# Performance work log

Hardware: AMD Instinct MI355X
Metric: run time of the kernel (lower is better)

Reference implementation:

```python
import jax, jax.numpy as jnp
import numpy as np

# SMPL constants
B, V, NJ, NB, NP, NJR = 256, 6890, 24, 10, 207, 43
PARENTS = np.array([0, 0, 0, 0, 1, 2, 3, 4, 5, 6, 7, 8, 9, 9, 9, 12, 13, 14, 16, 17, 18, 19, 20, 21])


def setup_inputs() -> dict:
    key = jax.random.key(0)
    ks = jax.random.split(key, 8)
    beta = jax.random.normal(ks[0], (B, NB), jnp.float32)
    theta = jax.random.normal(ks[1], (B, NJ * 3), jnp.float32)
    v_template = jax.random.normal(ks[2], (V, 3), jnp.float32)
    shapedirs = jax.random.normal(ks[3], (NB, V * 3), jnp.float32) * 0.01
    posedirs = jax.random.normal(ks[4], (NP, V * 3), jnp.float32) * 0.01
    jr = jax.random.uniform(ks[5], (NJ, V), jnp.float32)
    J_regressor = jr / jr.sum(axis=1, keepdims=True)
    jr2 = jax.random.uniform(ks[6], (NJR, V), jnp.float32)
    joint_regressor = jr2 / jr2.sum(axis=1, keepdims=True)
    w = jax.random.uniform(ks[7], (V, NJ), jnp.float32)
    w = w / w.sum(axis=1, keepdims=True)
    weights = jnp.broadcast_to(w[None], (B, V, NJ))  # tiled skinning weights, as in the torch buffer
    return dict(beta=beta, theta=theta, v_template=v_template, shapedirs=shapedirs,
                posedirs=posedirs, J_regressor=J_regressor,
                joint_regressor=joint_regressor, weights=weights)


def batch_rodrigues(theta):  # [N,3] axis-angle -> [N,3,3] rotation (via quaternion, HMR-style)
    angle = jnp.linalg.norm(theta + 1e-8, axis=1, keepdims=True)
    r = theta / angle
    half = angle * 0.5
    quat = jnp.concatenate([jnp.cos(half), jnp.sin(half) * r], axis=1)
    quat = quat / jnp.linalg.norm(quat, axis=1, keepdims=True)
    w, x, y, z = quat[:, 0], quat[:, 1], quat[:, 2], quat[:, 3]
    R = jnp.stack([
        1 - 2 * (y * y + z * z), 2 * (x * y - w * z), 2 * (x * z + w * y),
        2 * (x * y + w * z), 1 - 2 * (x * x + z * z), 2 * (y * z - w * x),
        2 * (x * z - w * y), 2 * (y * z + w * x), 1 - 2 * (x * x + y * y)], axis=1)
    return R.reshape(-1, 3, 3)


def batch_global_rigid_transformation(Rs, J):  # Rs [B,24,3,3], J [B,24,3]; rotate_base=True
    Rx = jnp.array([[1., 0., 0.], [0., -1., 0.], [0., 0., -1.]], dtype=Rs.dtype)
    root_R = jnp.matmul(Rs[:, 0], Rx)

    def make_A(R, t):  # [B,3,3],[B,3] -> [B,4,4]
        top = jnp.concatenate([R, t[:, :, None]], axis=2)
        bot = jnp.broadcast_to(jnp.array([0., 0., 0., 1.], dtype=R.dtype), (R.shape[0], 1, 4))
        return jnp.concatenate([top, bot], axis=1)

    res = [make_A(root_R, J[:, 0])]
    for i in range(1, NJ):  # fixed kinematic chain of 24 joints
        t = J[:, i] - J[:, PARENTS[i]]
        res.append(jnp.matmul(res[PARENTS[i]], make_A(Rs[:, i], t)))
    results = jnp.stack(res, axis=1)  # [B,24,4,4]
    J_transformed = results[:, :, :3, 3]
    Jh = jnp.concatenate([J, jnp.zeros_like(J[..., :1])], axis=-1)  # [B,24,4], w=0
    init_bone = jnp.einsum('bjmn,bjn->bjm', results, Jh)
    A = results - jnp.pad(init_bone[..., None], ((0, 0), (0, 0), (0, 0), (3, 0)))
    return J_transformed, A


def reference(beta, theta, v_template, shapedirs, posedirs, J_regressor, joint_regressor, weights):
    Bn = beta.shape[0]
    # shape blendshapes
    v_shaped = jnp.matmul(beta, shapedirs).reshape(Bn, V, 3) + v_template
    # joint locations from shaped mesh
    J = jnp.einsum('bvd,jv->bjd', v_shaped, J_regressor)  # [B,24,3]
    # pose rotations + pose blendshapes
    Rs = batch_rodrigues(theta.reshape(-1, 3)).reshape(Bn, NJ, 3, 3)
    pose_feature = (Rs[:, 1:] - jnp.eye(3, dtype=Rs.dtype)).reshape(Bn, NP)
    v_posed = jnp.matmul(pose_feature, posedirs).reshape(Bn, V, 3) + v_shaped
    # kinematic chain
    J_transformed, A = batch_global_rigid_transformation(Rs, J)
    # linear blend skinning
    T = jnp.einsum('bvj,bjmn->bvmn', weights, A)  # [B,V,4,4]
    vh = jnp.concatenate([v_posed, jnp.ones_like(v_posed[..., :1])], axis=-1)  # [B,V,4]
    verts = jnp.einsum('bvmn,bvn->bvm', T, vh)[..., :3]
    joints = jnp.einsum('bvd,jv->bjd', verts, joint_regressor)  # [B,43,3]
    return verts, joints
```

## Files before the change

### kernel.cpp

```cpp
#include <hip/hip_runtime.h>
#include <math.h>

#define B_   256
#define V_   6890
#define NJ_  24
#define NB_  10
#define NP_  207
#define NJR_ 43
#define V3_  20670
#define NK_  217
#define NJ3_ 129
#define JOUT_ 33024

#define JSTP_OFF 0
#define CG_OFF   8192
#define A_OFF    65536
#define JP_OFF   139264

__global__ __launch_bounds__(256) void k_jst(const float* __restrict__ JR,
                                             const float* __restrict__ vtm,
                                             const float* __restrict__ sd,
                                             float* __restrict__ JstP)
{
    const int j = blockIdx.x;
    const int c = blockIdx.y;
    const int tid = threadIdx.x;
    const int v0 = c * 862;
    const int v1 = (c == 7) ? V_ : v0 + 862;

    float acc[33];
#pragma unroll
    for (int q = 0; q < 33; q++) acc[q] = 0.f;

    for (int v = v0 + tid; v < v1; v += 256) {
        float jr = JR[(size_t)j * V_ + v];
        const float* tv = vtm + (size_t)v * 3;
        acc[0] += jr * tv[0];
        acc[1] += jr * tv[1];
        acc[2] += jr * tv[2];
#pragma unroll
        for (int k = 0; k < 10; k++) {
            const float* sp = sd + (size_t)k * V3_ + (size_t)v * 3;
            acc[3 + k*3 + 0] += jr * sp[0];
            acc[3 + k*3 + 1] += jr * sp[1];
            acc[3 + k*3 + 2] += jr * sp[2];
        }
    }
#pragma unroll
    for (int q = 0; q < 33; q++) {
        float s = acc[q];
#pragma unroll
        for (int off = 32; off > 0; off >>= 1) s += __shfl_xor(s, off);
        acc[q] = s;
    }
    __shared__ float red[4][33];
    const int wv = tid >> 6, ln = tid & 63;
    if (ln == 0) {
#pragma unroll
        for (int q = 0; q < 33; q++) red[wv][q] = acc[q];
    }
    __syncthreads();
    if (tid < 33)
        JstP[(c * 24 + j) * 33 + tid] =
            red[0][tid] + red[1][tid] + red[2][tid] + red[3][tid];
}

__global__ __launch_bounds__(64) void k_chain(const float* __restrict__ beta,
                                              const float* __restrict__ theta,
                                              const float* __restrict__ JstP,
                                              float* __restrict__ coefG,
                                              float* __restrict__ Aout)
{
    __shared__ float resL[24 * 12 * 64];
    __shared__ float JL[24 * 3 * 64];
    __shared__ float JstL[792];
    const int t = threadIdx.x;
    const int b = blockIdx.x * 64 + t;

    for (int i = t; i < 792; i += 64) {
        float s = 0.f;
#pragma unroll
        for (int c = 0; c < 8; c++) s += JstP[c * 792 + i];
        JstL[i] = s;
    }
    __syncthreads();

    float bet[10];
#pragma unroll
    for (int k = 0; k < 10; k++) bet[k] = beta[b * 10 + k];
#pragma unroll
    for (int k = 0; k < 10; k++) coefG[k * 256 + b] = bet[k];

#pragma unroll
    for (int j = 0; j < 24; j++) {
#pragma unroll
        for (int d = 0; d < 3; d++) {
            float s = JstL[j * 33 + d];
#pragma unroll
            for (int k = 0; k < 10; k++) s += bet[k] * JstL[j * 33 + 3 + k * 3 + d];
            JL[(j * 3 + d) * 64 + t] = s;
        }
    }

    const int par[24] = {0,0,0,0,1,2,3,4,5,6,7,8,9,9,9,12,13,14,16,17,18,19,20,21};

#pragma unroll
    for (int j = 0; j < 24; j++) {
        float t0 = theta[b * 72 + 3 * j + 0];
        float t1 = theta[b * 72 + 3 * j + 1];
        float t2 = theta[b * 72 + 3 * j + 2];
        float e0 = t0 + 1e-8f, e1 = t1 + 1e-8f, e2 = t2 + 1e-8f;
        float ang = sqrtf(e0 * e0 + e1 * e1 + e2 * e2);
        float inva = 1.0f / ang;
        float r0 = t0 * inva, r1 = t1 * inva, r2 = t2 * inva;
        float h = 0.5f * ang;
        float qw = cosf(h), sh = sinf(h);
        float qx = sh * r0, qy = sh * r1, qz = sh * r2;
        float qn = sqrtf(qw * qw + qx * qx + qy * qy + qz * qz);
        float inq = 1.0f / qn;
        qw *= inq; qx *= inq; qy *= inq; qz *= inq;
        float R[9];
        R[0] = 1.f - 2.f * (qy * qy + qz * qz);
        R[1] = 2.f * (qx * qy - qw * qz);
        R[2] = 2.f * (qx * qz + qw * qy);
        R[3] = 2.f * (qx * qy + qw * qz);
        R[4] = 1.f - 2.f * (qx * qx + qz * qz);
        R[5] = 2.f * (qy * qz - qw * qx);
        R[6] = 2.f * (qx * qz - qw * qy);
        R[7] = 2.f * (qy * qz + qw * qx);
        R[8] = 1.f - 2.f * (qx * qx + qy * qy);

        if (j == 0) {
#pragma unroll
            for (int m = 0; m < 3; m++) {
                resL[(0 * 12 + m * 4 + 0) * 64 + t] = R[m * 3 + 0];
                resL[(0 * 12 + m * 4 + 1) * 64 + t] = -R[m * 3 + 1];
                resL[(0 * 12 + m * 4 + 2) * 64 + t] = -R[m * 3 + 2];
                resL[(0 * 12 + m * 4 + 3) * 64 + t] = JL[(0 * 3 + m) * 64 + t];
            }
        } else {
#pragma unroll
            for (int e = 0; e < 9; e++)
                coefG[(10 + (j - 1) * 9 + e) * 256 + b] =
                    R[e] - ((e == 0 || e == 4 || e == 8) ? 1.f : 0.f);
            const int p = par[j];
            float tx = JL[(j * 3 + 0) * 64 + t] - JL[(p * 3 + 0) * 64 + t];
            float ty = JL[(j * 3 + 1) * 64 + t] - JL[(p * 3 + 1) * 64 + t];
            float tz = JL[(j * 3 + 2) * 64 + t] - JL[(p * 3 + 2) * 64 + t];
#pragma unroll
            for (int m = 0; m < 3; m++) {
                float pm0 = resL[(p * 12 + m * 4 + 0) * 64 + t];
                float pm1 = resL[(p * 12 + m * 4 + 1) * 64 + t];
                float pm2 = resL[(p * 12 + m * 4 + 2) * 64 + t];
                float pm3 = resL[(p * 12 + m * 4 + 3) * 64 + t];
                resL[(j * 12 + m * 4 + 0) * 64 + t] = pm0 * R[0] + pm1 * R[3] + pm2 * R[6];
                resL[(j * 12 + m * 4 + 1) * 64 + t] = pm0 * R[1] + pm1 * R[4] + pm2 * R[7];
                resL[(j * 12 + m * 4 + 2) * 64 + t] = pm0 * R[2] + pm1 * R[5] + pm2 * R[8];
                resL[(j * 12 + m * 4 + 3) * 64 + t] = pm0 * tx + pm1 * ty + pm2 * tz + pm3;
            }
        }
    }

#pragma unroll
    for (int j = 0; j < 24; j++) {
        float Jx = JL[(j * 3 + 0) * 64 + t];
        float Jy = JL[(j * 3 + 1) * 64 + t];
        float Jz = JL[(j * 3 + 2) * 64 + t];
#pragma unroll
        for (int m = 0; m < 3; m++) {
            float c0 = resL[(j * 12 + m * 4 + 0) * 64 + t];
            float c1 = resL[(j * 12 + m * 4 + 1) * 64 + t];
            float c2 = resL[(j * 12 + m * 4 + 2) * 64 + t];
            float c3 = resL[(j * 12 + m * 4 + 3) * 64 + t];
            float* ap = Aout + (size_t)(b * 24 + j) * 12 + m * 4;
            ap[0] = c0; ap[1] = c1; ap[2] = c2;
            ap[3] = c3 - (c0 * Jx + c1 * Jy + c2 * Jz);
        }
    }
}

__global__ __launch_bounds__(256) void k_vposed(const float* __restrict__ cg,
                                                const float* __restrict__ vt,
                                                const float* __restrict__ sd,
                                                const float* __restrict__ pd,
                                                float* __restrict__ vp)
{
    __shared__ __align__(16) float tile[64 * 32];
    const int tid  = threadIdx.x;
    const int cbase = blockIdx.x * 32;
    const bool tail = (cbase + 32 > V3_);
    const int b0  = (tid & 63) * 4;
    const int cg8 = tid >> 6;

    float acc[4][8];
#pragma unroll
    for (int i = 0; i < 4; i++)
#pragma unroll
        for (int j = 0; j < 8; j++) acc[i][j] = 0.f;

    for (int kb = 0; kb < NK_; kb += 64) {
        const int rows = (NK_ - kb < 64) ? (NK_ - kb) : 64;
        __syncthreads();
#pragma unroll
        for (int i = 0; i < 4; i++) {
            int s = tid + 256 * i;
            int r = s >> 4, c2 = (s & 15) * 2;
            if (r < rows) {
                int gr = kb + r;
                const float* src = ((gr < NB_) ? (sd + (size_t)gr * V3_)
                                               : (pd + (size_t)(gr - NB_) * V3_))
                                   + cbase + c2;
                float2 vv;
                if (!tail) {
                    vv = *(const float2*)src;
                } else {
                    vv.x = (cbase + c2     < V3_) ? src[0] : 0.f;
                    vv.y = (cbase + c2 + 1 < V3_) ? src[1] : 0.f;
                }
                *(float2*)(tile + r * 32 + c2) = vv;
            }
        }
        __syncthreads();
#pragma unroll 8
        for (int u = 0; u < rows; u++) {
            const float4 c4 = *(const float4*)(cg + (size_t)(kb + u) * 256 + b0);
            const float* rv = tile + u * 32 + cg8 * 8;
            const float4 vA = *(const float4*)(rv);
            const float4 vB = *(const float4*)(rv + 4);
            float ci[4] = {c4.x, c4.y, c4.z, c4.w};
            float vj[8] = {vA.x, vA.y, vA.z, vA.w, vB.x, vB.y, vB.z, vB.w};
#pragma unroll
            for (int i = 0; i < 4; i++)
#pragma unroll
                for (int j = 0; j < 8; j++) acc[i][j] += ci[i] * vj[j];
        }
    }

    const int col0 = cbase + cg8 * 8;
    if (!tail) {
        const float4 tA = *(const float4*)(vt + col0);
        const float4 tB = *(const float4*)(vt + col0 + 4);
        float tv[8] = {tA.x, tA.y, tA.z, tA.w, tB.x, tB.y, tB.z, tB.w};
#pragma unroll
        for (int i = 0; i < 4; i++) {
            float* o = vp + (size_t)(b0 + i) * V3_ + col0;
#pragma unroll
            for (int q = 0; q < 4; q++) {
                float2 st = {acc[i][2*q] + tv[2*q], acc[i][2*q+1] + tv[2*q+1]};
                *(float2*)(o + 2*q) = st;
            }
        }
    } else {
        float tv[8];
#pragma unroll
        for (int j = 0; j < 8; j++) tv[j] = (col0 + j < V3_) ? vt[col0 + j] : 0.f;
#pragma unroll
        for (int i = 0; i < 4; i++) {
            float* o = vp + (size_t)(b0 + i) * V3_ + col0;
#pragma unroll
            for (int j = 0; j < 8; j++)
                if (col0 + j < V3_) o[j] = acc[i][j] + tv[j];
        }
    }
}

__global__ __launch_bounds__(256) void k_skin(const float* __restrict__ w0,
                                              const float* __restrict__ A,
                                              float* __restrict__ verts)
{
    __shared__ __align__(16) float AL[288];
    const int tid = threadIdx.x;
    const int b = blockIdx.y;
    for (int i = tid; i < 288; i += 256) AL[i] = A[(size_t)b * 288 + i];
    __syncthreads();

#pragma unroll
    for (int rep = 0; rep < 2; rep++) {
        int v = blockIdx.x * 512 + rep * 256 + tid;
        if (v >= V_) continue;
        float wr[24];
        const float4* wp = (const float4*)(w0 + (size_t)v * 24);
#pragma unroll
        for (int q = 0; q < 6; q++) {
            float4 f = wp[q];
            wr[q * 4 + 0] = f.x; wr[q * 4 + 1] = f.y;
            wr[q * 4 + 2] = f.z; wr[q * 4 + 3] = f.w;
        }
        float T[12];
#pragma unroll
        for (int e = 0; e < 12; e++) T[e] = 0.f;
#pragma unroll
        for (int j = 0; j < 24; j++) {
            const float4* a4 = (const float4*)(AL + j * 12);
            float4 a0 = a4[0], a1 = a4[1], a2 = a4[2];
            float wj = wr[j];
            T[0] += wj * a0.x; T[1] += wj * a0.y; T[2]  += wj * a0.z; T[3]  += wj * a0.w;
            T[4] += wj * a1.x; T[5] += wj * a1.y; T[6]  += wj * a1.z; T[7]  += wj * a1.w;
            T[8] += wj * a2.x; T[9] += wj * a2.y; T[10] += wj * a2.z; T[11] += wj * a2.w;
        }
        float* pv = verts + (size_t)b * V3_ + (size_t)v * 3;
        float p0 = pv[0], p1 = pv[1], p2 = pv[2];
        pv[0] = T[0] * p0 + T[1] * p1 + T[2]  * p2 + T[3];
        pv[1] = T[4] * p0 + T[5] * p1 + T[6]  * p2 + T[7];
        pv[2] = T[8] * p0 + T[9] * p1 + T[10] * p2 + T[11];
    }
}

__global__ __launch_bounds__(256) void k_joints(const float* __restrict__ jreg,
                                                const float* __restrict__ verts,
                                                float* __restrict__ jp)
{
    const int tid = threadIdx.x;
    const int b0 = blockIdx.x * 4;
    const int jr0 = blockIdx.y * 8;
    const int z = blockIdx.z;
    const int v0 = z * 1723;
    const int v1 = (z == 3) ? V_ : v0 + 1723;

    float acc[96];
#pragma unroll
    for (int c = 0; c < 96; c++) acc[c] = 0.f;

    for (int v = v0 + tid; v < v1; v += 256) {
        float jr[8];
#pragma unroll
        for (int q = 0; q < 8; q++) {
            int j = jr0 + q;
            jr[q] = (j < NJR_) ? jreg[(size_t)j * V_ + v] : 0.f;
        }
#pragma unroll
        for (int i = 0; i < 4; i++) {
            const float* pv = verts + (size_t)(b0 + i) * V3_ + (size_t)v * 3;
            float p0 = pv[0], p1 = pv[1], p2 = pv[2];
#pragma unroll
            for (int q = 0; q < 8; q++) {
                acc[q * 12 + i * 3 + 0] += jr[q] * p0;
                acc[q * 12 + i * 3 + 1] += jr[q] * p1;
                acc[q * 12 + i * 3 + 2] += jr[q] * p2;
            }
        }
    }
#pragma unroll
    for (int c = 0; c < 96; c++) {
        float s = acc[c];
#pragma unroll
        for (int off = 32; off > 0; off >>= 1) s += __shfl_xor(s, off);
        acc[c] = s;
    }
    __shared__ float red[4][96];
    const int wv = tid >> 6, ln = tid & 63;
    if (ln == 0) {
#pragma unroll
        for (int c = 0; c < 96; c++) red[wv][c] = acc[c];
    }
    __syncthreads();
    if (tid < 96) {
        float s = red[0][tid] + red[1][tid] + red[2][tid] + red[3][tid];
        int q = tid / 12, rem = tid % 12, i2 = rem / 3, d = rem % 3;
        int j = jr0 + q;
        if (j < NJR_)
            jp[(size_t)z * JOUT_ + (b0 + i2) * NJ3_ + j * 3 + d] = s;
    }
}

__global__ __launch_bounds__(256) void k_jfinal(const float* __restrict__ jp,
                                                float* __restrict__ joints)
{
    int i = blockIdx.x * 256 + threadIdx.x;
    if (i < JOUT_)
        joints[i] = jp[i] + jp[JOUT_ + i] + jp[2 * JOUT_ + i] + jp[3 * JOUT_ + i];
}

extern "C" void kernel_launch(void* const* d_in, const int* in_sizes, int n_in,
                              void* d_out, int out_size, void* d_ws, size_t ws_size,
                              hipStream_t stream)
{
    const float* beta  = (const float*)d_in[0];
    const float* theta = (const float*)d_in[1];
    const float* vtm   = (const float*)d_in[2];
    const float* sd    = (const float*)d_in[3];
    const float* pd    = (const float*)d_in[4];
    const float* JR    = (const float*)d_in[5];
    const float* jreg  = (const float*)d_in[6];
    const float* wts   = (const float*)d_in[7];

    float* out = (float*)d_out;
    float* ws  = (float*)d_ws;
    float* JstP = ws + JSTP_OFF;
    float* cg   = ws + CG_OFF;
    float* A    = ws + A_OFF;
    float* jp   = ws + JP_OFF;
    float* verts  = out;
    float* joints = out + (size_t)B_ * V3_;

    hipLaunchKernelGGL(k_jst,    dim3(24, 8),    dim3(256), 0, stream, JR, vtm, sd, JstP);
    hipLaunchKernelGGL(k_chain,  dim3(4),        dim3(64),  0, stream, beta, theta, JstP, cg, A);
    hipLaunchKernelGGL(k_vposed, dim3(646),      dim3(256), 0, stream, cg, vtm, sd, pd, verts);
    hipLaunchKernelGGL(k_skin,   dim3(14, 256),  dim3(256), 0, stream, wts, A, verts);
    hipLaunchKernelGGL(k_joints, dim3(64, 6, 4), dim3(256), 0, stream, jreg, verts, jp);
    hipLaunchKernelGGL(k_jfinal, dim3(129),      dim3(256), 0, stream, jp, joints);
}
```

Before: 399.1 us.

## Restructure joint-regression and kinematic-chain kernels for wider parallelism

k_jst now runs one block per vertex chunk (16 chunks), with 8 lanes per joint reduced by a short shuffle, instead of 24x8 blocks each doing full-block reductions. k_chain moves from 4 blocks of 64 threads (one batch element per thread) to 16 blocks of 256 threads, with 16 threads cooperating per batch element on the 3x4 transform entries, and a barrier after each joint. k_joints processes 11 regressor rows per block instead of 8, cutting grid y from 6 to 4 and reducing re-reads of verts. The costs are more registers in k_joints, less per-element parallel work in k_jst, and 24 serial barriers in k_chain.

```diff
diff --git a/kernel.cpp b/kernel.cpp
--- a/kernel.cpp
+++ b/kernel.cpp
@@ -11,28 +11,30 @@
 #define NK_  217
 #define NJ3_ 129
 #define JOUT_ 33024
+#define NCH_ 16
 
 #define JSTP_OFF 0
-#define CG_OFF   8192
-#define A_OFF    65536
-#define JP_OFF   139264
-
-__global__ __launch_bounds__(256) void k_jst(const float* __restrict__ JR,
+#define CG_OFF   16384
+#define A_OFF    73728
+#define JP_OFF   147456
+
+__global__ __launch_bounds__(192) void k_jst(const float* __restrict__ JR,
                                              const float* __restrict__ vtm,
                                              const float* __restrict__ sd,
                                              float* __restrict__ JstP)
 {
-    const int j = blockIdx.x;
-    const int c = blockIdx.y;
+    const int c = blockIdx.x;
     const int tid = threadIdx.x;
-    const int v0 = c * 862;
-    const int v1 = (c == 7) ? V_ : v0 + 862;
+    const int j = tid >> 3;
+    const int s = tid & 7;
+    const int v0 = c * 431;
+    const int v1 = (v0 + 431 < V_) ? v0 + 431 : V_;
 
     float acc[33];
 #pragma unroll
     for (int q = 0; q < 33; q++) acc[q] = 0.f;
 
-    for (int v = v0 + tid; v < v1; v += 256) {
+    for (int v = v0 + s; v < v1; v += 8) {
         float jr = JR[(size_t)j * V_ + v];
         const float* tv = vtm + (size_t)v * 3;
         acc[0] += jr * tv[0];
@@ -48,67 +50,65 @@
     }
 #pragma unroll
     for (int q = 0; q < 33; q++) {
-        float s = acc[q];
-#pragma unroll
-        for (int off = 32; off > 0; off >>= 1) s += __shfl_xor(s, off);
-        acc[q] = s;
-    }
-    __shared__ float red[4][33];
-    const int wv = tid >> 6, ln = tid & 63;
-    if (ln == 0) {
-#pragma unroll
-        for (int q = 0; q < 33; q++) red[wv][q] = acc[q];
+        float t = acc[q];
+        t += __shfl_xor(t, 1);
+        t += __shfl_xor(t, 2);
+        t += __shfl_xor(t, 4);
+        acc[q] = t;
+    }
+    if (s == 0) {
+        float* dst = JstP + (c * 24 + j) * 33;
+#pragma unroll
+        for (int q = 0; q < 33; q++) dst[q] = acc[q];
+    }
+}
+
+#define RES_STRIDE 292
+__global__ __launch_bounds__(256) void k_chain(const float* __restrict__ beta,
+                                               const float* __restrict__ theta,
+                                               const float* __restrict__ JstP,
+                                               float* __restrict__ coefG,
+                                               float* __restrict__ Aout)
+{
+    __shared__ float JstL[792];
+    __shared__ float JL[16 * 72];
+    __shared__ float resL[16 * RES_STRIDE];
+    const int tid = threadIdx.x;
+    const int bl = tid >> 4;
+    const int e  = tid & 15;
+    const int b  = blockIdx.x * 16 + bl;
+    const int m  = e >> 2, n = e & 3;
+
+    for (int i = tid; i < 792; i += 256) {
+        float s = 0.f;
+#pragma unroll
+        for (int c = 0; c < NCH_; c++) s += JstP[c * 792 + i];
+        JstL[i] = s;
     }
     __syncthreads();
-    if (tid < 33)
-        JstP[(c * 24 + j) * 33 + tid] =
-            red[0][tid] + red[1][tid] + red[2][tid] + red[3][tid];
-}
-
-__global__ __launch_bounds__(64) void k_chain(const float* __restrict__ beta,
-                                              const float* __restrict__ theta,
-                                              const float* __restrict__ JstP,
-                                              float* __restrict__ coefG,
-                                              float* __restrict__ Aout)
-{
-    __shared__ float resL[24 * 12 * 64];
-    __shared__ float JL[24 * 3 * 64];
-    __shared__ float JstL[792];
-    const int t = threadIdx.x;
-    const int b = blockIdx.x * 64 + t;
-
-    for (int i = t; i < 792; i += 64) {
-        float s = 0.f;
-#pragma unroll
-        for (int c = 0; c < 8; c++) s += JstP[c * 792 + i];
-        JstL[i] = s;
+
+    for (int idx = tid; idx < 1152; idx += 256) {
+        int bb = idx / 72, rem = idx % 72;
+        int jj = rem / 3, d = rem % 3;
+        const float* bp = beta + (size_t)(blockIdx.x * 16 + bb) * 10;
+        float s = JstL[jj * 33 + d];
+#pragma unroll
+        for (int k = 0; k < 10; k++) s += bp[k] * JstL[jj * 33 + 3 + k * 3 + d];
+        JL[bb * 72 + rem] = s;
+    }
+    for (int idx = tid; idx < 160; idx += 256) {
+        int bb = idx & 15, k = idx >> 4;
+        int gb = blockIdx.x * 16 + bb;
+        coefG[k * 256 + gb] = beta[(size_t)gb * 10 + k];
     }
     __syncthreads();
 
-    float bet[10];
-#pragma unroll
-    for (int k = 0; k < 10; k++) bet[k] = beta[b * 10 + k];
-#pragma unroll
-    for (int k = 0; k < 10; k++) coefG[k * 256 + b] = bet[k];
-
-#pragma unroll
+    const int par[24] = {0,0,0,0,1,2,3,4,5,6,7,8,9,9,9,12,13,14,16,17,18,19,20,21};
+
     for (int j = 0; j < 24; j++) {
-#pragma unroll
-        for (int d = 0; d < 3; d++) {
-            float s = JstL[j * 33 + d];
-#pragma unroll
-            for (int k = 0; k < 10; k++) s += bet[k] * JstL[j * 33 + 3 + k * 3 + d];
-            JL[(j * 3 + d) * 64 + t] = s;
-        }
-    }
-
-    const int par[24] = {0,0,0,0,1,2,3,4,5,6,7,8,9,9,9,12,13,14,16,17,18,19,20,21};
-
-#pragma unroll
-    for (int j = 0; j < 24; j++) {
-        float t0 = theta[b * 72 + 3 * j + 0];
-        float t1 = theta[b * 72 + 3 * j + 1];
-        float t2 = theta[b * 72 + 3 * j + 2];
+        float t0 = theta[(size_t)b * 72 + 3 * j + 0];
+        float t1 = theta[(size_t)b * 72 + 3 * j + 1];
+        float t2 = theta[(size_t)b * 72 + 3 * j + 2];
         float e0 = t0 + 1e-8f, e1 = t1 + 1e-8f, e2 = t2 + 1e-8f;
         float ang = sqrtf(e0 * e0 + e1 * e1 + e2 * e2);
         float inva = 1.0f / ang;
@@ -116,8 +116,7 @@
         float h = 0.5f * ang;
         float qw = cosf(h), sh = sinf(h);
         float qx = sh * r0, qy = sh * r1, qz = sh * r2;
-        float qn = sqrtf(qw * qw + qx * qx + qy * qy + qz * qz);
-        float inq = 1.0f / qn;
+        float inq = 1.0f / sqrtf(qw * qw + qx * qx + qy * qy + qz * qz);
         qw *= inq; qx *= inq; qy *= inq; qz *= inq;
         float R[9];
         R[0] = 1.f - 2.f * (qy * qy + qz * qz);
@@ -131,50 +130,48 @@
         R[8] = 1.f - 2.f * (qx * qx + qy * qy);
 
         if (j == 0) {
-#pragma unroll
-            for (int m = 0; m < 3; m++) {
-                resL[(0 * 12 + m * 4 + 0) * 64 + t] = R[m * 3 + 0];
-                resL[(0 * 12 + m * 4 + 1) * 64 + t] = -R[m * 3 + 1];
-                resL[(0 * 12 + m * 4 + 2) * 64 + t] = -R[m * 3 + 2];
-                resL[(0 * 12 + m * 4 + 3) * 64 + t] = JL[(0 * 3 + m) * 64 + t];
+            if (e < 12) {
+                float val;
+                if (n < 3) val = R[m * 3 + n] * ((n == 0) ? 1.f : -1.f);
+                else       val = JL[bl * 72 + 0 * 3 + m];
+                resL[bl * RES_STRIDE + 0 * 12 + e] = val;
             }
         } else {
-#pragma unroll
-            for (int e = 0; e < 9; e++)
+            if (e < 9)
                 coefG[(10 + (j - 1) * 9 + e) * 256 + b] =
                     R[e] - ((e == 0 || e == 4 || e == 8) ? 1.f : 0.f);
             const int p = par[j];
-            float tx = JL[(j * 3 + 0) * 64 + t] - JL[(p * 3 + 0) * 64 + t];
-            float ty = JL[(j * 3 + 1) * 64 + t] - JL[(p * 3 + 1) * 64 + t];
-            float tz = JL[(j * 3 + 2) * 64 + t] - JL[(p * 3 + 2) * 64 + t];
-#pragma unroll
-            for (int m = 0; m < 3; m++) {
-                float pm0 = resL[(p * 12 + m * 4 + 0) * 64 + t];
-                float pm1 = resL[(p * 12 + m * 4 + 1) * 64 + t];
-                float pm2 = resL[(p * 12 + m * 4 + 2) * 64 + t];
-                float pm3 = resL[(p * 12 + m * 4 + 3) * 64 + t];
-                resL[(j * 12 + m * 4 + 0) * 64 + t] = pm0 * R[0] + pm1 * R[3] + pm2 * R[6];
-                resL[(j * 12 + m * 4 + 1) * 64 + t] = pm0 * R[1] + pm1 * R[4] + pm2 * R[7];
-                resL[(j * 12 + m * 4 + 2) * 64 + t] = pm0 * R[2] + pm1 * R[5] + pm2 * R[8];
-                resL[(j * 12 + m * 4 + 3) * 64 + t] = pm0 * tx + pm1 * ty + pm2 * tz + pm3;
-            }
-        }
-    }
-
-#pragma unroll
-    for (int j = 0; j < 24; j++) {
-        float Jx = JL[(j * 3 + 0) * 64 + t];
-        float Jy = JL[(j * 3 + 1) * 64 + t];
-        float Jz = JL[(j * 3 + 2) * 64 + t];
-#pragma unroll
-        for (int m = 0; m < 3; m++) {
-            float c0 = resL[(j * 12 + m * 4 + 0) * 64 + t];
-            float c1 = resL[(j * 12 + m * 4 + 1) * 64 + t];
-            float c2 = resL[(j * 12 + m * 4 + 2) * 64 + t];
-            float c3 = resL[(j * 12 + m * 4 + 3) * 64 + t];
-            float* ap = Aout + (size_t)(b * 24 + j) * 12 + m * 4;
-            ap[0] = c0; ap[1] = c1; ap[2] = c2;
-            ap[3] = c3 - (c0 * Jx + c1 * Jy + c2 * Jz);
+            if (e < 12) {
+                const float* pr = resL + bl * RES_STRIDE + p * 12 + m * 4;
+                float pm0 = pr[0], pm1 = pr[1], pm2 = pr[2], pm3 = pr[3];
+                float val;
+                if (n < 3) {
+                    val = pm0 * R[n] + pm1 * R[3 + n] + pm2 * R[6 + n];
+                } else {
+                    float tx = JL[bl * 72 + j * 3 + 0] - JL[bl * 72 + p * 3 + 0];
+                    float ty = JL[bl * 72 + j * 3 + 1] - JL[bl * 72 + p * 3 + 1];
+                    float tz = JL[bl * 72 + j * 3 + 2] - JL[bl * 72 + p * 3 + 2];
+                    val = pm0 * tx + pm1 * ty + pm2 * tz + pm3;
+                }
+                resL[bl * RES_STRIDE + j * 12 + e] = val;
+            }
+        }
+        __syncthreads();
+    }
+
+    if (e < 12) {
+        for (int j = 0; j < 24; j++) {
+            const float* rr = resL + bl * RES_STRIDE + j * 12 + m * 4;
+            float val;
+            if (n < 3) {
+                val = rr[n];
+            } else {
+                float Jx = JL[bl * 72 + j * 3 + 0];
+                float Jy = JL[bl * 72 + j * 3 + 1];
+                float Jz = JL[bl * 72 + j * 3 + 2];
+                val = rr[3] - (rr[0] * Jx + rr[1] * Jy + rr[2] * Jz);
+            }
+            Aout[(size_t)(b * 24 + j) * 12 + e] = val;
         }
     }
 }
@@ -312,19 +309,19 @@
 {
     const int tid = threadIdx.x;
     const int b0 = blockIdx.x * 4;
-    const int jr0 = blockIdx.y * 8;
+    const int jr0 = blockIdx.y * 11;
     const int z = blockIdx.z;
     const int v0 = z * 1723;
     const int v1 = (z == 3) ? V_ : v0 + 1723;
 
-    float acc[96];
-#pragma unroll
-    for (int c = 0; c < 96; c++) acc[c] = 0.f;
+    float acc[132];
+#pragma unroll
+    for (int c = 0; c < 132; c++) acc[c] = 0.f;
 
     for (int v = v0 + tid; v < v1; v += 256) {
-        float jr[8];
-#pragma unroll
-        for (int q = 0; q < 8; q++) {
+        float jr[11];
+#pragma unroll
+        for (int q = 0; q < 11; q++) {
             int j = jr0 + q;
             jr[q] = (j < NJR_) ? jreg[(size_t)j * V_ + v] : 0.f;
         }
@@ -333,7 +330,7 @@
             const float* pv = verts + (size_t)(b0 + i) * V3_ + (size_t)v * 3;
             float p0 = pv[0], p1 = pv[1], p2 = pv[2];
 #pragma unroll
-            for (int q = 0; q < 8; q++) {
+            for (int q = 0; q < 11; q++) {
                 acc[q * 12 + i * 3 + 0] += jr[q] * p0;
                 acc[q * 12 + i * 3 + 1] += jr[q] * p1;
                 acc[q * 12 + i * 3 + 2] += jr[q] * p2;
@@ -341,20 +338,20 @@
         }
     }
 #pragma unroll
-    for (int c = 0; c < 96; c++) {
+    for (int c = 0; c < 132; c++) {
         float s = acc[c];
 #pragma unroll
         for (int off = 32; off > 0; off >>= 1) s += __shfl_xor(s, off);
         acc[c] = s;
     }
-    __shared__ float red[4][96];
+    __shared__ float red[4][132];
     const int wv = tid >> 6, ln = tid & 63;
     if (ln == 0) {
 #pragma unroll
-        for (int c = 0; c < 96; c++) red[wv][c] = acc[c];
+        for (int c = 0; c < 132; c++) red[wv][c] = acc[c];
     }
     __syncthreads();
-    if (tid < 96) {
+    if (tid < 132) {
         float s = red[0][tid] + red[1][tid] + red[2][tid] + red[3][tid];
         int q = tid / 12, rem = tid % 12, i2 = rem / 3, d = rem % 3;
         int j = jr0 + q;
@@ -393,10 +390,10 @@
     float* verts  = out;
     float* joints = out + (size_t)B_ * V3_;
 
-    hipLaunchKernelGGL(k_jst,    dim3(24, 8),    dim3(256), 0, stream, JR, vtm, sd, JstP);
-    hipLaunchKernelGGL(k_chain,  dim3(4),        dim3(64),  0, stream, beta, theta, JstP, cg, A);
+    hipLaunchKernelGGL(k_jst,    dim3(NCH_),     dim3(192), 0, stream, JR, vtm, sd, JstP);
+    hipLaunchKernelGGL(k_chain,  dim3(16),       dim3(256), 0, stream, beta, theta, JstP, cg, A);
     hipLaunchKernelGGL(k_vposed, dim3(646),      dim3(256), 0, stream, cg, vtm, sd, pd, verts);
     hipLaunchKernelGGL(k_skin,   dim3(14, 256),  dim3(256), 0, stream, wts, A, verts);
-    hipLaunchKernelGGL(k_joints, dim3(64, 6, 4), dim3(256), 0, stream, jreg, verts, jp);
+    hipLaunchKernelGGL(k_joints, dim3(64, 4, 4), dim3(256), 0, stream, jreg, verts, jp);
     hipLaunchKernelGGL(k_jfinal, dim3(129),      dim3(256), 0, stream, jp, joints);
 }
```

After: 444.6 us. +11.4%, slower.
